# Performance work log

Measured on AMD Instinct MI355X. Metric: run time of the kernel, lower is better.

Reference implementation:

```python
import jax, jax.numpy as jnp
import numpy as np
from jax import lax

DISCOUNT = 0.99
NORMALIZE = True
EPS = 1e-9


def setup_inputs() -> dict:
    key = jax.random.key(0)
    k1, k2 = jax.random.split(key)
    B, T = 4096, 8192
    rewards = jax.random.normal(k1, (B, T), dtype=jnp.float32)
    done_flags = (jax.random.uniform(k2, (B, T)) < 0.01).astype(jnp.float32)
    return {"rewards": rewards, "done_flags": done_flags}


def _episode_returns(rewards, done_flags):
    # reverse-time recurrence: r_t = rew_t + gamma * r_{t+1} * (1 - done_t)
    rw = jnp.moveaxis(rewards, -1, 0)      # [T, B]
    dn = jnp.moveaxis(done_flags, -1, 0)   # [T, B]

    def step(carry, xs):
        r, d = xs
        ret = r + DISCOUNT * carry * (1.0 - d)
        return ret, ret

    # init carry = 0 makes the last step reduce to returns[-1] = rewards[-1]
    _, rets = lax.scan(step, jnp.zeros_like(rw[0]), (rw, dn), reverse=True)
    returns = jnp.moveaxis(rets, 0, -1)    # [B, T]

    if NORMALIZE:
        # torch: (returns - returns.mean()) / (returns.std(dim=-1) + 1e-9)
        # global mean, per-trajectory std (unbiased, matching torch default)
        std = jnp.std(returns, axis=-1, ddof=1, keepdims=True)
        returns = (returns - jnp.mean(returns)) / (std + EPS)
    return returns


def reference(rewards, done_flags):
    return _episode_returns(rewards, done_flags)
```

## Files before the change

### kernel.cpp

```cpp
#include <hip/hip_runtime.h>
#include <math.h>

#define TLEN   8192
#define BROWS  4096
#define NT     256
#define TILE   2048
#define CHUNK  8
#define NTILES (TLEN / TILE)
#define GAMMA  0.99f
#define EPSN   1e-9

typedef float f4 __attribute__((ext_vector_type(4)));

__global__ __launch_bounds__(NT) void er_scan(const float* __restrict__ rew,
                                              const float* __restrict__ don,
                                              float* __restrict__ out,
                                              double* __restrict__ rowSum,
                                              float* __restrict__ rowInv) {
  __shared__ float  wgA[NTILES][4];
  __shared__ float  wgP[NTILES][4];
  __shared__ double red[8];

  const int row  = blockIdx.x;
  const int tid  = threadIdx.x;
  const int lane = tid & 63;
  const int wv   = tid >> 6;
  const size_t rbase = (size_t)row * TLEN;

  const f4* gr = (const f4*)(rew + rbase);
  const f4* gd = (const f4*)(don + rbase);

  f4 r0, r1, d0, d1;
  {
    const int f = (NTILES - 1) * (TILE / 4) + 2 * tid;
    r0 = gr[f]; r1 = gr[f + 1];
    d0 = gd[f]; d1 = gd[f + 1];
  }

  double accS = 0.0, accQ = 0.0;
  float  tc = 0.f;

  for (int k = NTILES - 1; k >= 0; --k) {
    const bool more = (k > 0);
    f4 pr0, pr1, pd0, pd1;
    if (more) {
      const int f = (k - 1) * (TILE / 4) + 2 * tid;
      pr0 = gr[f]; pr1 = gr[f + 1];
      pd0 = gd[f]; pd1 = gd[f + 1];
    }

    float rv[CHUNK], cv[CHUNK];
    rv[0] = r0.x; rv[1] = r0.y; rv[2] = r0.z; rv[3] = r0.w;
    rv[4] = r1.x; rv[5] = r1.y; rv[6] = r1.z; rv[7] = r1.w;
    cv[0] = fmaf(-GAMMA, d0.x, GAMMA);
    cv[1] = fmaf(-GAMMA, d0.y, GAMMA);
    cv[2] = fmaf(-GAMMA, d0.z, GAMMA);
    cv[3] = fmaf(-GAMMA, d0.w, GAMMA);
    cv[4] = fmaf(-GAMMA, d1.x, GAMMA);
    cv[5] = fmaf(-GAMMA, d1.y, GAMMA);
    cv[6] = fmaf(-GAMMA, d1.z, GAMMA);
    cv[7] = fmaf(-GAMMA, d1.w, GAMMA);

    float A = 0.f, P = 1.f;
#pragma unroll
    for (int j = CHUNK - 1; j >= 0; --j) {
      A = fmaf(cv[j], A, rv[j]);
      P *= cv[j];
      rv[j] = A;
      cv[j] = P;
    }

    float sA = A, sP = P;
#pragma unroll
    for (int d = 1; d < 64; d <<= 1) {
      const float tA = __shfl_down(sA, d);
      const float tP = __shfl_down(sP, d);
      if (lane + d < 64) { sA = fmaf(sP, tA, sA); sP *= tP; }
    }
    if (lane == 0) { wgA[k][wv] = sA; wgP[k][wv] = sP; }
    __syncthreads();

    float wc = tc;
#pragma unroll
    for (int j = 3; j >= 1; --j) {
      const float nw = fmaf(wgP[k][j], wc, wgA[k][j]);
      wc = (j > wv) ? nw : wc;
    }
    float tcn = tc;
#pragma unroll
    for (int j = 3; j >= 0; --j) tcn = fmaf(wgP[k][j], tcn, wgA[k][j]);

    float eA = __shfl_down(sA, 1);
    float eP = __shfl_down(sP, 1);
    if (lane == 63) { eA = 0.f; eP = 1.f; }
    const float carry = fmaf(eP, wc, eA);

    float fsum = 0.f, fsq = 0.f;
    float o[CHUNK];
#pragma unroll
    for (int j = 0; j < CHUNK; ++j) {
      const float r = fmaf(cv[j], carry, rv[j]);
      o[j] = r;
      fsum += r;
      fsq  = fmaf(r, r, fsq);
    }
    f4* go = (f4*)(out + rbase + (size_t)k * TILE + (size_t)tid * CHUNK);
    f4 o0; o0.x = o[0]; o0.y = o[1]; o0.z = o[2]; o0.w = o[3];
    f4 o1; o1.x = o[4]; o1.y = o[5]; o1.z = o[6]; o1.w = o[7];
    go[0] = o0;
    go[1] = o1;
    accS += (double)fsum;
    accQ += (double)fsq;
    tc = tcn;

    if (more) { r0 = pr0; r1 = pr1; d0 = pd0; d1 = pd1; }
  }

  double ds = accS, dq = accQ;
#pragma unroll
  for (int d = 32; d >= 1; d >>= 1) {
    ds += __shfl_down(ds, d);
    dq += __shfl_down(dq, d);
  }
  if (lane == 0) { red[wv] = ds; red[4 + wv] = dq; }
  __syncthreads();
  if (tid == 0) {
    const double s = red[0] + red[1] + red[2] + red[3];
    const double q = red[4] + red[5] + red[6] + red[7];
    rowSum[row] = s;
    double var = (q - s * s / (double)TLEN) / (double)(TLEN - 1);
    if (var < 0.0) var = 0.0;
    rowInv[row] = (float)(1.0 / (sqrt(var) + EPSN));
  }
}

__global__ __launch_bounds__(256) void er_mean(const double* __restrict__ rowSum,
                                               float* __restrict__ meanPtr) {
  const int tid = threadIdx.x;
  double s = 0.0;
  for (int i = tid; i < BROWS; i += 256) s += rowSum[i];
#pragma unroll
  for (int d = 32; d >= 1; d >>= 1) s += __shfl_down(s, d);
  __shared__ double red[4];
  const int lane = tid & 63, wv = tid >> 6;
  if (lane == 0) red[wv] = s;
  __syncthreads();
  if (tid == 0) {
    const double t = red[0] + red[1] + red[2] + red[3];
    *meanPtr = (float)(t / ((double)BROWS * (double)TLEN));
  }
}

#define K3_BLOCKS 2048
__global__ __launch_bounds__(256) void er_norm(float* __restrict__ out,
                                               const float* __restrict__ rowInv,
                                               const float* __restrict__ meanPtr) {
  const float mean = *meanPtr;
  const unsigned total4 = (unsigned)BROWS * (TLEN / 4);
  const unsigned stride = K3_BLOCKS * 256;
  f4* o4 = (f4*)out;
  for (unsigned i = blockIdx.x * 256 + threadIdx.x; i < total4; i += stride) {
    const int row = (int)(i >> 11);
    const float inv = rowInv[row];
    f4 v = o4[i];
    v.x = (v.x - mean) * inv;
    v.y = (v.y - mean) * inv;
    v.z = (v.z - mean) * inv;
    v.w = (v.w - mean) * inv;
    __builtin_nontemporal_store(v, o4 + i);
  }
}

extern "C" void kernel_launch(void* const* d_in, const int* in_sizes, int n_in,
                              void* d_out, int out_size, void* d_ws, size_t ws_size,
                              hipStream_t stream) {
  const float* rew = (const float*)d_in[0];
  const float* don = (const float*)d_in[1];
  float* out = (float*)d_out;

  double* rowSum  = (double*)d_ws;
  float*  rowInv  = (float*)((char*)d_ws + BROWS * 8);
  float*  meanPtr = (float*)((char*)d_ws + BROWS * 8 + BROWS * 4);

  er_scan<<<BROWS, NT, 0, stream>>>(rew, don, out, rowSum, rowInv);
  er_mean<<<1, 256, 0, stream>>>(rowSum, meanPtr);
  er_norm<<<K3_BLOCKS, 256, 0, stream>>>(out, rowInv, meanPtr);
}
```

Measured before the change: 361.0 us.

## Load whole row upfront and scan all tiles with single barrier

The scan kernel now loads all four tiles of a row into registers at once and computes the local and wave-level scans for every tile independently. The four per-tile barriers are replaced by one barrier followed by a serial combine over 16 wave aggregates. This removes the tile-to-tile serial dependency and exposes more memory-level parallelism, at the cost of much higher register use and possibly lower occupancy. The normalize kernel also switches from nontemporal stores to ordinary stores.

```diff
diff --git a/kernel.cpp b/kernel.cpp
--- a/kernel.cpp
+++ b/kernel.cpp
@@ -5,7 +5,6 @@
 #define BROWS  4096
 #define NT     256
 #define TILE   2048
-#define CHUNK  8
 #define NTILES (TLEN / TILE)
 #define GAMMA  0.99f
 #define EPSN   1e-9
@@ -17,8 +16,7 @@
                                               float* __restrict__ out,
                                               double* __restrict__ rowSum,
                                               float* __restrict__ rowInv) {
-  __shared__ float  wgA[NTILES][4];
-  __shared__ float  wgP[NTILES][4];
+  __shared__ float  sAl[16], sPl[16];
   __shared__ double red[8];
 
   const int row  = blockIdx.x;
@@ -30,90 +28,93 @@
   const f4* gr = (const f4*)(rew + rbase);
   const f4* gd = (const f4*)(don + rbase);
 
-  f4 r0, r1, d0, d1;
-  {
-    const int f = (NTILES - 1) * (TILE / 4) + 2 * tid;
-    r0 = gr[f]; r1 = gr[f + 1];
-    d0 = gd[f]; d1 = gd[f + 1];
+  f4 R[8], D[8];
+#pragma unroll
+  for (int k = 0; k < NTILES; ++k) {
+    const int f = k * (TILE / 4) + 2 * tid;
+    R[2 * k]     = gr[f];
+    R[2 * k + 1] = gr[f + 1];
+    D[2 * k]     = gd[f];
+    D[2 * k + 1] = gd[f + 1];
+  }
+
+  float rv[32], cv[32];
+#pragma unroll
+  for (int k = 0; k < NTILES; ++k) {
+    const f4 r0 = R[2 * k], r1 = R[2 * k + 1];
+    const f4 d0 = D[2 * k], d1 = D[2 * k + 1];
+    rv[8 * k + 0] = r0.x; rv[8 * k + 1] = r0.y; rv[8 * k + 2] = r0.z; rv[8 * k + 3] = r0.w;
+    rv[8 * k + 4] = r1.x; rv[8 * k + 5] = r1.y; rv[8 * k + 6] = r1.z; rv[8 * k + 7] = r1.w;
+    cv[8 * k + 0] = fmaf(-GAMMA, d0.x, GAMMA);
+    cv[8 * k + 1] = fmaf(-GAMMA, d0.y, GAMMA);
+    cv[8 * k + 2] = fmaf(-GAMMA, d0.z, GAMMA);
+    cv[8 * k + 3] = fmaf(-GAMMA, d0.w, GAMMA);
+    cv[8 * k + 4] = fmaf(-GAMMA, d1.x, GAMMA);
+    cv[8 * k + 5] = fmaf(-GAMMA, d1.y, GAMMA);
+    cv[8 * k + 6] = fmaf(-GAMMA, d1.z, GAMMA);
+    cv[8 * k + 7] = fmaf(-GAMMA, d1.w, GAMMA);
+  }
+
+#pragma unroll
+  for (int k = 0; k < NTILES; ++k) {
+    float A = 0.f, P = 1.f;
+#pragma unroll
+    for (int j = 7; j >= 0; --j) {
+      const int i = 8 * k + j;
+      A = fmaf(cv[i], A, rv[i]);
+      P *= cv[i];
+      rv[i] = A;
+      cv[i] = P;
+    }
+  }
+
+  float eA[4], eP[4];
+#pragma unroll
+  for (int k = 0; k < NTILES; ++k) {
+    float sA = rv[8 * k], sP = cv[8 * k];
+#pragma unroll
+    for (int d = 1; d < 64; d <<= 1) {
+      const float uA = __shfl_down(sA, d);
+      const float uP = __shfl_down(sP, d);
+      if (lane + d < 64) { sA = fmaf(sP, uA, sA); sP *= uP; }
+    }
+    if (lane == 0) { sAl[4 * k + wv] = sA; sPl[4 * k + wv] = sP; }
+    const float xA = __shfl_down(sA, 1);
+    const float xP = __shfl_down(sP, 1);
+    eA[k] = (lane == 63) ? 0.f : xA;
+    eP[k] = (lane == 63) ? 1.f : xP;
+  }
+
+  __syncthreads();
+
+  float wc[4];
+  float x = 0.f;
+#pragma unroll
+  for (int m = 15; m >= 0; --m) {
+    if ((m & 3) == wv) wc[m >> 2] = x;
+    x = fmaf(sPl[m], x, sAl[m]);
   }
 
   double accS = 0.0, accQ = 0.0;
-  float  tc = 0.f;
-
-  for (int k = NTILES - 1; k >= 0; --k) {
-    const bool more = (k > 0);
-    f4 pr0, pr1, pd0, pd1;
-    if (more) {
-      const int f = (k - 1) * (TILE / 4) + 2 * tid;
-      pr0 = gr[f]; pr1 = gr[f + 1];
-      pd0 = gd[f]; pd1 = gd[f + 1];
-    }
-
-    float rv[CHUNK], cv[CHUNK];
-    rv[0] = r0.x; rv[1] = r0.y; rv[2] = r0.z; rv[3] = r0.w;
-    rv[4] = r1.x; rv[5] = r1.y; rv[6] = r1.z; rv[7] = r1.w;
-    cv[0] = fmaf(-GAMMA, d0.x, GAMMA);
-    cv[1] = fmaf(-GAMMA, d0.y, GAMMA);
-    cv[2] = fmaf(-GAMMA, d0.z, GAMMA);
-    cv[3] = fmaf(-GAMMA, d0.w, GAMMA);
-    cv[4] = fmaf(-GAMMA, d1.x, GAMMA);
-    cv[5] = fmaf(-GAMMA, d1.y, GAMMA);
-    cv[6] = fmaf(-GAMMA, d1.z, GAMMA);
-    cv[7] = fmaf(-GAMMA, d1.w, GAMMA);
-
-    float A = 0.f, P = 1.f;
 #pragma unroll
-    for (int j = CHUNK - 1; j >= 0; --j) {
-      A = fmaf(cv[j], A, rv[j]);
-      P *= cv[j];
-      rv[j] = A;
-      cv[j] = P;
-    }
-
-    float sA = A, sP = P;
+  for (int k = 0; k < NTILES; ++k) {
+    const float carry = fmaf(eP[k], wc[k], eA[k]);
+    float fsum = 0.f, fsq = 0.f;
+    float o[8];
 #pragma unroll
-    for (int d = 1; d < 64; d <<= 1) {
-      const float tA = __shfl_down(sA, d);
-      const float tP = __shfl_down(sP, d);
-      if (lane + d < 64) { sA = fmaf(sP, tA, sA); sP *= tP; }
-    }
-    if (lane == 0) { wgA[k][wv] = sA; wgP[k][wv] = sP; }
-    __syncthreads();
-
-    float wc = tc;
-#pragma unroll
-    for (int j = 3; j >= 1; --j) {
-      const float nw = fmaf(wgP[k][j], wc, wgA[k][j]);
-      wc = (j > wv) ? nw : wc;
-    }
-    float tcn = tc;
-#pragma unroll
-    for (int j = 3; j >= 0; --j) tcn = fmaf(wgP[k][j], tcn, wgA[k][j]);
-
-    float eA = __shfl_down(sA, 1);
-    float eP = __shfl_down(sP, 1);
-    if (lane == 63) { eA = 0.f; eP = 1.f; }
-    const float carry = fmaf(eP, wc, eA);
-
-    float fsum = 0.f, fsq = 0.f;
-    float o[CHUNK];
-#pragma unroll
-    for (int j = 0; j < CHUNK; ++j) {
-      const float r = fmaf(cv[j], carry, rv[j]);
+    for (int j = 0; j < 8; ++j) {
+      const float r = fmaf(cv[8 * k + j], carry, rv[8 * k + j]);
       o[j] = r;
       fsum += r;
       fsq  = fmaf(r, r, fsq);
     }
-    f4* go = (f4*)(out + rbase + (size_t)k * TILE + (size_t)tid * CHUNK);
+    f4* go = (f4*)(out + rbase + (size_t)k * TILE) + 2 * tid;
     f4 o0; o0.x = o[0]; o0.y = o[1]; o0.z = o[2]; o0.w = o[3];
     f4 o1; o1.x = o[4]; o1.y = o[5]; o1.z = o[6]; o1.w = o[7];
     go[0] = o0;
     go[1] = o1;
     accS += (double)fsum;
     accQ += (double)fsq;
-    tc = tcn;
-
-    if (more) { r0 = pr0; r1 = pr1; d0 = pd0; d1 = pd1; }
   }
 
   double ds = accS, dq = accQ;
@@ -167,7 +168,7 @@
     v.y = (v.y - mean) * inv;
     v.z = (v.z - mean) * inv;
     v.w = (v.w - mean) * inv;
-    __builtin_nontemporal_store(v, o4 + i);
+    o4[i] = v;
   }
 }
 
```

Result: no change. 361.6 us (+0.2%).

## Fuse scan, mean, and normalize into one persistent kernel with grid barrier

Applied to the files above, without the earlier changes.

Replaces the three-kernel pipeline with a single persistent kernel of 1024 blocks, each handling 4 rows. A global atomic sum plus a spin-wait counter barrier supplies the global mean, and per-row inverse std is kept in LDS. Each block then normalizes its own rows in place, so the extra launches go away and the normalize pass can read rows a block just wrote while they may still be in cache. The risks are that correctness depends on all 1024 blocks being co-resident (otherwise the spin-wait only ends at its iteration cap), the barrier adds idle time, and each block now walks its rows one after another, which lowers parallelism.

```diff
diff --git a/kernel.cpp b/kernel.cpp
--- a/kernel.cpp
+++ b/kernel.cpp
@@ -9,165 +9,167 @@
 #define NTILES (TLEN / TILE)
 #define GAMMA  0.99f
 #define EPSN   1e-9
+#define GRID   1024
+#define RPB    (BROWS / GRID)
 
 typedef float f4 __attribute__((ext_vector_type(4)));
 
-__global__ __launch_bounds__(NT) void er_scan(const float* __restrict__ rew,
-                                              const float* __restrict__ don,
-                                              float* __restrict__ out,
-                                              double* __restrict__ rowSum,
-                                              float* __restrict__ rowInv) {
-  __shared__ float  wgA[NTILES][4];
-  __shared__ float  wgP[NTILES][4];
+__global__ __launch_bounds__(NT, 4) void er_fused(const float* __restrict__ rew,
+                                                  const float* __restrict__ don,
+                                                  float* __restrict__ out,
+                                                  double* __restrict__ tsum,
+                                                  unsigned* __restrict__ counter) {
+  __shared__ float  wgA[NTILES][4], wgP[NTILES][4];
   __shared__ double red[8];
+  __shared__ float  invLds[RPB];
+  __shared__ float  meanLds;
 
-  const int row  = blockIdx.x;
   const int tid  = threadIdx.x;
   const int lane = tid & 63;
   const int wv   = tid >> 6;
-  const size_t rbase = (size_t)row * TLEN;
+  const int row0 = blockIdx.x * RPB;
 
-  const f4* gr = (const f4*)(rew + rbase);
-  const f4* gd = (const f4*)(don + rbase);
+  double bsum = 0.0;
 
-  f4 r0, r1, d0, d1;
-  {
-    const int f = (NTILES - 1) * (TILE / 4) + 2 * tid;
-    r0 = gr[f]; r1 = gr[f + 1];
-    d0 = gd[f]; d1 = gd[f + 1];
+  for (int rr = 0; rr < RPB; ++rr) {
+    const size_t rbase = (size_t)(row0 + rr) * TLEN;
+    const f4* gr = (const f4*)(rew + rbase);
+    const f4* gd = (const f4*)(don + rbase);
+
+    f4 r0, r1, d0, d1;
+    {
+      const int f = (NTILES - 1) * (TILE / 4) + 2 * tid;
+      r0 = gr[f]; r1 = gr[f + 1];
+      d0 = gd[f]; d1 = gd[f + 1];
+    }
+
+    double accS = 0.0, accQ = 0.0;
+    float  tc = 0.f;
+
+    for (int k = NTILES - 1; k >= 0; --k) {
+      const bool more = (k > 0);
+      f4 pr0, pr1, pd0, pd1;
+      if (more) {
+        const int f = (k - 1) * (TILE / 4) + 2 * tid;
+        pr0 = gr[f]; pr1 = gr[f + 1];
+        pd0 = gd[f]; pd1 = gd[f + 1];
+      }
+
+      float rv[CHUNK], cv[CHUNK];
+      rv[0] = r0.x; rv[1] = r0.y; rv[2] = r0.z; rv[3] = r0.w;
+      rv[4] = r1.x; rv[5] = r1.y; rv[6] = r1.z; rv[7] = r1.w;
+      cv[0] = fmaf(-GAMMA, d0.x, GAMMA);
+      cv[1] = fmaf(-GAMMA, d0.y, GAMMA);
+      cv[2] = fmaf(-GAMMA, d0.z, GAMMA);
+      cv[3] = fmaf(-GAMMA, d0.w, GAMMA);
+      cv[4] = fmaf(-GAMMA, d1.x, GAMMA);
+      cv[5] = fmaf(-GAMMA, d1.y, GAMMA);
+      cv[6] = fmaf(-GAMMA, d1.z, GAMMA);
+      cv[7] = fmaf(-GAMMA, d1.w, GAMMA);
+
+      float A = 0.f, P = 1.f;
+#pragma unroll
+      for (int j = CHUNK - 1; j >= 0; --j) {
+        A = fmaf(cv[j], A, rv[j]);
+        P *= cv[j];
+        rv[j] = A;
+        cv[j] = P;
+      }
+
+      float sA = A, sP = P;
+#pragma unroll
+      for (int d = 1; d < 64; d <<= 1) {
+        const float tA = __shfl_down(sA, d);
+        const float tP = __shfl_down(sP, d);
+        if (lane + d < 64) { sA = fmaf(sP, tA, sA); sP *= tP; }
+      }
+      if (lane == 0) { wgA[k][wv] = sA; wgP[k][wv] = sP; }
+      __syncthreads();
+
+      float wc = tc;
+#pragma unroll
+      for (int j = 3; j >= 1; --j) {
+        const float nw = fmaf(wgP[k][j], wc, wgA[k][j]);
+        wc = (j > wv) ? nw : wc;
+      }
+      float tcn = tc;
+#pragma unroll
+      for (int j = 3; j >= 0; --j) tcn = fmaf(wgP[k][j], tcn, wgA[k][j]);
+
+      float eA = __shfl_down(sA, 1);
+      float eP = __shfl_down(sP, 1);
+      if (lane == 63) { eA = 0.f; eP = 1.f; }
+      const float carry = fmaf(eP, wc, eA);
+
+      float fsum = 0.f, fsq = 0.f;
+      float o[CHUNK];
+#pragma unroll
+      for (int j = 0; j < CHUNK; ++j) {
+        const float r = fmaf(cv[j], carry, rv[j]);
+        o[j] = r;
+        fsum += r;
+        fsq  = fmaf(r, r, fsq);
+      }
+      f4* go = (f4*)(out + rbase + (size_t)k * TILE) + 2 * tid;
+      f4 o0; o0.x = o[0]; o0.y = o[1]; o0.z = o[2]; o0.w = o[3];
+      f4 o1; o1.x = o[4]; o1.y = o[5]; o1.z = o[6]; o1.w = o[7];
+      go[0] = o0;
+      go[1] = o1;
+      accS += (double)fsum;
+      accQ += (double)fsq;
+      tc = tcn;
+
+      if (more) { r0 = pr0; r1 = pr1; d0 = pd0; d1 = pd1; }
+    }
+
+    double ds = accS, dq = accQ;
+#pragma unroll
+    for (int d = 32; d >= 1; d >>= 1) {
+      ds += __shfl_down(ds, d);
+      dq += __shfl_down(dq, d);
+    }
+    if (lane == 0) { red[wv] = ds; red[4 + wv] = dq; }
+    __syncthreads();
+    if (tid == 0) {
+      const double s = red[0] + red[1] + red[2] + red[3];
+      const double q = red[4] + red[5] + red[6] + red[7];
+      bsum += s;
+      double var = (q - s * s / (double)TLEN) / (double)(TLEN - 1);
+      if (var < 0.0) var = 0.0;
+      invLds[rr] = (float)(1.0 / (sqrt(var) + EPSN));
+    }
   }
 
-  double accS = 0.0, accQ = 0.0;
-  float  tc = 0.f;
+  if (tid == 0) {
+    atomicAdd(tsum, bsum);
+    __threadfence();
+    atomicAdd(counter, 1u);
+    unsigned it = 0;
+    while (__hip_atomic_load(counter, __ATOMIC_ACQUIRE, __HIP_MEMORY_SCOPE_AGENT) < GRID) {
+      __builtin_amdgcn_s_sleep(32);
+      if (++it > (1u << 22)) break;
+    }
+    const unsigned long long rawv =
+        __hip_atomic_load((unsigned long long*)tsum, __ATOMIC_RELAXED,
+                          __HIP_MEMORY_SCOPE_AGENT);
+    const double t = __builtin_bit_cast(double, rawv);
+    meanLds = (float)(t / ((double)BROWS * (double)TLEN));
+  }
+  __syncthreads();
+  const float mean = meanLds;
 
-  for (int k = NTILES - 1; k >= 0; --k) {
-    const bool more = (k > 0);
-    f4 pr0, pr1, pd0, pd1;
-    if (more) {
-      const int f = (k - 1) * (TILE / 4) + 2 * tid;
-      pr0 = gr[f]; pr1 = gr[f + 1];
-      pd0 = gd[f]; pd1 = gd[f + 1];
+  for (int rr = 0; rr < RPB; ++rr) {
+    const float inv = invLds[rr];
+    f4* o4 = (f4*)(out + (size_t)(row0 + rr) * TLEN);
+#pragma unroll
+    for (int i = tid; i < TLEN / 4; i += NT) {
+      f4 v = o4[i];
+      v.x = (v.x - mean) * inv;
+      v.y = (v.y - mean) * inv;
+      v.z = (v.z - mean) * inv;
+      v.w = (v.w - mean) * inv;
+      o4[i] = v;
     }
-
-    float rv[CHUNK], cv[CHUNK];
-    rv[0] = r0.x; rv[1] = r0.y; rv[2] = r0.z; rv[3] = r0.w;
-    rv[4] = r1.x; rv[5] = r1.y; rv[6] = r1.z; rv[7] = r1.w;
-    cv[0] = fmaf(-GAMMA, d0.x, GAMMA);
-    cv[1] = fmaf(-GAMMA, d0.y, GAMMA);
-    cv[2] = fmaf(-GAMMA, d0.z, GAMMA);
-    cv[3] = fmaf(-GAMMA, d0.w, GAMMA);
-    cv[4] = fmaf(-GAMMA, d1.x, GAMMA);
-    cv[5] = fmaf(-GAMMA, d1.y, GAMMA);
-    cv[6] = fmaf(-GAMMA, d1.z, GAMMA);
-    cv[7] = fmaf(-GAMMA, d1.w, GAMMA);
-
-    float A = 0.f, P = 1.f;
-#pragma unroll
-    for (int j = CHUNK - 1; j >= 0; --j) {
-      A = fmaf(cv[j], A, rv[j]);
-      P *= cv[j];
-      rv[j] = A;
-      cv[j] = P;
-    }
-
-    float sA = A, sP = P;
-#pragma unroll
-    for (int d = 1; d < 64; d <<= 1) {
-      const float tA = __shfl_down(sA, d);
-      const float tP = __shfl_down(sP, d);
-      if (lane + d < 64) { sA = fmaf(sP, tA, sA); sP *= tP; }
-    }
-    if (lane == 0) { wgA[k][wv] = sA; wgP[k][wv] = sP; }
-    __syncthreads();
-
-    float wc = tc;
-#pragma unroll
-    for (int j = 3; j >= 1; --j) {
-      const float nw = fmaf(wgP[k][j], wc, wgA[k][j]);
-      wc = (j > wv) ? nw : wc;
-    }
-    float tcn = tc;
-#pragma unroll
-    for (int j = 3; j >= 0; --j) tcn = fmaf(wgP[k][j], tcn, wgA[k][j]);
-
-    float eA = __shfl_down(sA, 1);
-    float eP = __shfl_down(sP, 1);
-    if (lane == 63) { eA = 0.f; eP = 1.f; }
-    const float carry = fmaf(eP, wc, eA);
-
-    float fsum = 0.f, fsq = 0.f;
-    float o[CHUNK];
-#pragma unroll
-    for (int j = 0; j < CHUNK; ++j) {
-      const float r = fmaf(cv[j], carry, rv[j]);
-      o[j] = r;
-      fsum += r;
-      fsq  = fmaf(r, r, fsq);
-    }
-    f4* go = (f4*)(out + rbase + (size_t)k * TILE + (size_t)tid * CHUNK);
-    f4 o0; o0.x = o[0]; o0.y = o[1]; o0.z = o[2]; o0.w = o[3];
-    f4 o1; o1.x = o[4]; o1.y = o[5]; o1.z = o[6]; o1.w = o[7];
-    go[0] = o0;
-    go[1] = o1;
-    accS += (double)fsum;
-    accQ += (double)fsq;
-    tc = tcn;
-
-    if (more) { r0 = pr0; r1 = pr1; d0 = pd0; d1 = pd1; }
-  }
-
-  double ds = accS, dq = accQ;
-#pragma unroll
-  for (int d = 32; d >= 1; d >>= 1) {
-    ds += __shfl_down(ds, d);
-    dq += __shfl_down(dq, d);
-  }
-  if (lane == 0) { red[wv] = ds; red[4 + wv] = dq; }
-  __syncthreads();
-  if (tid == 0) {
-    const double s = red[0] + red[1] + red[2] + red[3];
-    const double q = red[4] + red[5] + red[6] + red[7];
-    rowSum[row] = s;
-    double var = (q - s * s / (double)TLEN) / (double)(TLEN - 1);
-    if (var < 0.0) var = 0.0;
-    rowInv[row] = (float)(1.0 / (sqrt(var) + EPSN));
-  }
-}
-
-__global__ __launch_bounds__(256) void er_mean(const double* __restrict__ rowSum,
-                                               float* __restrict__ meanPtr) {
-  const int tid = threadIdx.x;
-  double s = 0.0;
-  for (int i = tid; i < BROWS; i += 256) s += rowSum[i];
-#pragma unroll
-  for (int d = 32; d >= 1; d >>= 1) s += __shfl_down(s, d);
-  __shared__ double red[4];
-  const int lane = tid & 63, wv = tid >> 6;
-  if (lane == 0) red[wv] = s;
-  __syncthreads();
-  if (tid == 0) {
-    const double t = red[0] + red[1] + red[2] + red[3];
-    *meanPtr = (float)(t / ((double)BROWS * (double)TLEN));
-  }
-}
-
-#define K3_BLOCKS 2048
-__global__ __launch_bounds__(256) void er_norm(float* __restrict__ out,
-                                               const float* __restrict__ rowInv,
-                                               const float* __restrict__ meanPtr) {
-  const float mean = *meanPtr;
-  const unsigned total4 = (unsigned)BROWS * (TLEN / 4);
-  const unsigned stride = K3_BLOCKS * 256;
-  f4* o4 = (f4*)out;
-  for (unsigned i = blockIdx.x * 256 + threadIdx.x; i < total4; i += stride) {
-    const int row = (int)(i >> 11);
-    const float inv = rowInv[row];
-    f4 v = o4[i];
-    v.x = (v.x - mean) * inv;
-    v.y = (v.y - mean) * inv;
-    v.z = (v.z - mean) * inv;
-    v.w = (v.w - mean) * inv;
-    __builtin_nontemporal_store(v, o4 + i);
   }
 }
 
@@ -178,11 +180,9 @@
   const float* don = (const float*)d_in[1];
   float* out = (float*)d_out;
 
-  double* rowSum  = (double*)d_ws;
-  float*  rowInv  = (float*)((char*)d_ws + BROWS * 8);
-  float*  meanPtr = (float*)((char*)d_ws + BROWS * 8 + BROWS * 4);
+  double*   tsum    = (double*)d_ws;
+  unsigned* counter = (unsigned*)((char*)d_ws + 8);
 
-  er_scan<<<BROWS, NT, 0, stream>>>(rew, don, out, rowSum, rowInv);
-  er_mean<<<1, 256, 0, stream>>>(rowSum, meanPtr);
-  er_norm<<<K3_BLOCKS, 256, 0, stream>>>(out, rowInv, meanPtr);
+  hipMemsetAsync(d_ws, 0, 16, stream);
+  er_fused<<<GRID, NT, 0, stream>>>(rew, don, out, tsum, counter);
 }
```

New measurement: 622.4 us. +72.4%, slower.

## Assign one wavefront per row, removing block barriers, and double-buffer tile loads

Applied to the files above, without the earlier changes.

The scan kernel now gives each 64-lane wavefront a whole row, stepping backward through 512-element tiles. Tile prefixes are combined with wave shuffles instead of shared-memory exchanges and __syncthreads. Loads are double-buffered across two register sets, separated by sched barriers, to overlap memory with the serial scan. The normalization kernel now uses one block per row with plain stores instead of nontemporal ones. The serial chain per row is longer (16 tiles per wave), which relies on more resident waves to hide latency.

```diff
diff --git a/kernel.cpp b/kernel.cpp
--- a/kernel.cpp
+++ b/kernel.cpp
@@ -4,116 +4,119 @@
 #define TLEN   8192
 #define BROWS  4096
 #define NT     256
-#define TILE   2048
-#define CHUNK  8
-#define NTILES (TLEN / TILE)
+#define WPB    (NT / 64)
+#define GRID   (BROWS / WPB)
+#define TPW    512
+#define NTW    (TLEN / TPW)
 #define GAMMA  0.99f
 #define EPSN   1e-9
 
 typedef float f4 __attribute__((ext_vector_type(4)));
 
-__global__ __launch_bounds__(NT) void er_scan(const float* __restrict__ rew,
-                                              const float* __restrict__ don,
-                                              float* __restrict__ out,
-                                              double* __restrict__ rowSum,
-                                              float* __restrict__ rowInv) {
-  __shared__ float  wgA[NTILES][4];
-  __shared__ float  wgP[NTILES][4];
-  __shared__ double red[8];
+__device__ __forceinline__ void scan_tile(const f4 r0, const f4 r1,
+                                          const f4 d0, const f4 d1,
+                                          const int lane, float& tc,
+                                          float* __restrict__ dst,
+                                          double& accS, double& accQ) {
+  float rv[8], cv[8];
+  rv[0] = r0.x; rv[1] = r0.y; rv[2] = r0.z; rv[3] = r0.w;
+  rv[4] = r1.x; rv[5] = r1.y; rv[6] = r1.z; rv[7] = r1.w;
+  cv[0] = fmaf(-GAMMA, d0.x, GAMMA);
+  cv[1] = fmaf(-GAMMA, d0.y, GAMMA);
+  cv[2] = fmaf(-GAMMA, d0.z, GAMMA);
+  cv[3] = fmaf(-GAMMA, d0.w, GAMMA);
+  cv[4] = fmaf(-GAMMA, d1.x, GAMMA);
+  cv[5] = fmaf(-GAMMA, d1.y, GAMMA);
+  cv[6] = fmaf(-GAMMA, d1.z, GAMMA);
+  cv[7] = fmaf(-GAMMA, d1.w, GAMMA);
 
-  const int row  = blockIdx.x;
+  float A = 0.f, P = 1.f;
+#pragma unroll
+  for (int j = 7; j >= 0; --j) {
+    A = fmaf(cv[j], A, rv[j]);
+    P *= cv[j];
+    rv[j] = A;
+    cv[j] = P;
+  }
+
+  float sA = A, sP = P;
+#pragma unroll
+  for (int d = 1; d < 64; d <<= 1) {
+    const float tA = __shfl_down(sA, d);
+    const float tP = __shfl_down(sP, d);
+    if (lane + d < 64) { sA = fmaf(sP, tA, sA); sP *= tP; }
+  }
+
+  float eA = __shfl_down(sA, 1);
+  float eP = __shfl_down(sP, 1);
+  if (lane == 63) { eA = 0.f; eP = 1.f; }
+  const float carry = fmaf(eP, tc, eA);
+
+  const float gA = __shfl(sA, 0);
+  const float gP = __shfl(sP, 0);
+  tc = fmaf(gP, tc, gA);
+
+  float fs = 0.f, fq = 0.f;
+  float o[8];
+#pragma unroll
+  for (int j = 0; j < 8; ++j) {
+    const float r = fmaf(cv[j], carry, rv[j]);
+    o[j] = r;
+    fs += r;
+    fq  = fmaf(r, r, fq);
+  }
+  f4* go = (f4*)dst + 2 * lane;
+  f4 o0; o0.x = o[0]; o0.y = o[1]; o0.z = o[2]; o0.w = o[3];
+  f4 o1; o1.x = o[4]; o1.y = o[5]; o1.z = o[6]; o1.w = o[7];
+  go[0] = o0;
+  go[1] = o1;
+  accS += (double)fs;
+  accQ += (double)fq;
+}
+
+__global__ __launch_bounds__(NT, 4) void er_scan(const float* __restrict__ rew,
+                                                 const float* __restrict__ don,
+                                                 float* __restrict__ out,
+                                                 double* __restrict__ rowSum,
+                                                 float* __restrict__ rowInv) {
   const int tid  = threadIdx.x;
   const int lane = tid & 63;
   const int wv   = tid >> 6;
+  const int row  = blockIdx.x * WPB + wv;
   const size_t rbase = (size_t)row * TLEN;
 
   const f4* gr = (const f4*)(rew + rbase);
   const f4* gd = (const f4*)(don + rbase);
+  float* ob = out + rbase;
 
-  f4 r0, r1, d0, d1;
+  f4 aR0, aR1, aD0, aD1, bR0, bR1, bD0, bD1;
   {
-    const int f = (NTILES - 1) * (TILE / 4) + 2 * tid;
-    r0 = gr[f]; r1 = gr[f + 1];
-    d0 = gd[f]; d1 = gd[f + 1];
+    const int f = (NTW - 1) * (TPW / 4) + 2 * lane;
+    aR0 = gr[f]; aR1 = gr[f + 1];
+    aD0 = gd[f]; aD1 = gd[f + 1];
   }
 
+  float tc = 0.f;
   double accS = 0.0, accQ = 0.0;
-  float  tc = 0.f;
 
-  for (int k = NTILES - 1; k >= 0; --k) {
-    const bool more = (k > 0);
-    f4 pr0, pr1, pd0, pd1;
-    if (more) {
-      const int f = (k - 1) * (TILE / 4) + 2 * tid;
-      pr0 = gr[f]; pr1 = gr[f + 1];
-      pd0 = gd[f]; pd1 = gd[f + 1];
+#pragma unroll
+  for (int kk = 0; kk < NTW / 2; ++kk) {
+    const int k = NTW - 1 - 2 * kk;
+    if (k >= 1) {
+      const int f = (k - 1) * (TPW / 4) + 2 * lane;
+      bR0 = gr[f]; bR1 = gr[f + 1];
+      bD0 = gd[f]; bD1 = gd[f + 1];
     }
+    __builtin_amdgcn_sched_barrier(0);
+    scan_tile(aR0, aR1, aD0, aD1, lane, tc, ob + (size_t)k * TPW, accS, accQ);
 
-    float rv[CHUNK], cv[CHUNK];
-    rv[0] = r0.x; rv[1] = r0.y; rv[2] = r0.z; rv[3] = r0.w;
-    rv[4] = r1.x; rv[5] = r1.y; rv[6] = r1.z; rv[7] = r1.w;
-    cv[0] = fmaf(-GAMMA, d0.x, GAMMA);
-    cv[1] = fmaf(-GAMMA, d0.y, GAMMA);
-    cv[2] = fmaf(-GAMMA, d0.z, GAMMA);
-    cv[3] = fmaf(-GAMMA, d0.w, GAMMA);
-    cv[4] = fmaf(-GAMMA, d1.x, GAMMA);
-    cv[5] = fmaf(-GAMMA, d1.y, GAMMA);
-    cv[6] = fmaf(-GAMMA, d1.z, GAMMA);
-    cv[7] = fmaf(-GAMMA, d1.w, GAMMA);
-
-    float A = 0.f, P = 1.f;
-#pragma unroll
-    for (int j = CHUNK - 1; j >= 0; --j) {
-      A = fmaf(cv[j], A, rv[j]);
-      P *= cv[j];
-      rv[j] = A;
-      cv[j] = P;
+    if (k >= 2) {
+      const int f = (k - 2) * (TPW / 4) + 2 * lane;
+      aR0 = gr[f]; aR1 = gr[f + 1];
+      aD0 = gd[f]; aD1 = gd[f + 1];
     }
-
-    float sA = A, sP = P;
-#pragma unroll
-    for (int d = 1; d < 64; d <<= 1) {
-      const float tA = __shfl_down(sA, d);
-      const float tP = __shfl_down(sP, d);
-      if (lane + d < 64) { sA = fmaf(sP, tA, sA); sP *= tP; }
-    }
-    if (lane == 0) { wgA[k][wv] = sA; wgP[k][wv] = sP; }
-    __syncthreads();
-
-    float wc = tc;
-#pragma unroll
-    for (int j = 3; j >= 1; --j) {
-      const float nw = fmaf(wgP[k][j], wc, wgA[k][j]);
-      wc = (j > wv) ? nw : wc;
-    }
-    float tcn = tc;
-#pragma unroll
-    for (int j = 3; j >= 0; --j) tcn = fmaf(wgP[k][j], tcn, wgA[k][j]);
-
-    float eA = __shfl_down(sA, 1);
-    float eP = __shfl_down(sP, 1);
-    if (lane == 63) { eA = 0.f; eP = 1.f; }
-    const float carry = fmaf(eP, wc, eA);
-
-    float fsum = 0.f, fsq = 0.f;
-    float o[CHUNK];
-#pragma unroll
-    for (int j = 0; j < CHUNK; ++j) {
-      const float r = fmaf(cv[j], carry, rv[j]);
-      o[j] = r;
-      fsum += r;
-      fsq  = fmaf(r, r, fsq);
-    }
-    f4* go = (f4*)(out + rbase + (size_t)k * TILE + (size_t)tid * CHUNK);
-    f4 o0; o0.x = o[0]; o0.y = o[1]; o0.z = o[2]; o0.w = o[3];
-    f4 o1; o1.x = o[4]; o1.y = o[5]; o1.z = o[6]; o1.w = o[7];
-    go[0] = o0;
-    go[1] = o1;
-    accS += (double)fsum;
-    accQ += (double)fsq;
-    tc = tcn;
-
-    if (more) { r0 = pr0; r1 = pr1; d0 = pd0; d1 = pd1; }
+    __builtin_amdgcn_sched_barrier(0);
+    scan_tile(bR0, bR1, bD0, bD1, lane, tc, ob + (size_t)(k - 1) * TPW, accS, accQ);
   }
 
   double ds = accS, dq = accQ;
@@ -122,13 +125,9 @@
     ds += __shfl_down(ds, d);
     dq += __shfl_down(dq, d);
   }
-  if (lane == 0) { red[wv] = ds; red[4 + wv] = dq; }
-  __syncthreads();
-  if (tid == 0) {
-    const double s = red[0] + red[1] + red[2] + red[3];
-    const double q = red[4] + red[5] + red[6] + red[7];
-    rowSum[row] = s;
-    double var = (q - s * s / (double)TLEN) / (double)(TLEN - 1);
+  if (lane == 0) {
+    rowSum[row] = ds;
+    double var = (dq - ds * ds / (double)TLEN) / (double)(TLEN - 1);
     if (var < 0.0) var = 0.0;
     rowInv[row] = (float)(1.0 / (sqrt(var) + EPSN));
   }
@@ -151,23 +150,21 @@
   }
 }
 
-#define K3_BLOCKS 2048
 __global__ __launch_bounds__(256) void er_norm(float* __restrict__ out,
                                                const float* __restrict__ rowInv,
                                                const float* __restrict__ meanPtr) {
+  const int row = blockIdx.x;
   const float mean = *meanPtr;
-  const unsigned total4 = (unsigned)BROWS * (TLEN / 4);
-  const unsigned stride = K3_BLOCKS * 256;
-  f4* o4 = (f4*)out;
-  for (unsigned i = blockIdx.x * 256 + threadIdx.x; i < total4; i += stride) {
-    const int row = (int)(i >> 11);
-    const float inv = rowInv[row];
+  const float inv  = rowInv[row];
+  f4* o4 = (f4*)(out + (size_t)row * TLEN);
+#pragma unroll
+  for (int i = threadIdx.x; i < TLEN / 4; i += 256) {
     f4 v = o4[i];
     v.x = (v.x - mean) * inv;
     v.y = (v.y - mean) * inv;
     v.z = (v.z - mean) * inv;
     v.w = (v.w - mean) * inv;
-    __builtin_nontemporal_store(v, o4 + i);
+    o4[i] = v;
   }
 }
 
@@ -182,7 +179,7 @@
   float*  rowInv  = (float*)((char*)d_ws + BROWS * 8);
   float*  meanPtr = (float*)((char*)d_ws + BROWS * 8 + BROWS * 4);
 
-  er_scan<<<BROWS, NT, 0, stream>>>(rew, don, out, rowSum, rowInv);
+  er_scan<<<GRID, NT, 0, stream>>>(rew, don, out, rowSum, rowInv);
   er_mean<<<1, 256, 0, stream>>>(rowSum, meanPtr);
-  er_norm<<<K3_BLOCKS, 256, 0, stream>>>(out, rowInv, meanPtr);
+  er_norm<<<BROWS, 256, 0, stream>>>(out, rowInv, meanPtr);
 }
```

After: 354.7 us. About the same (-1.7%).
